# Kernel tuning notes

Hardware: AMD Instinct MI355X
Metric: run time of the kernel (lower is better)

Reference implementation:

```python
import jax, jax.numpy as jnp
import numpy as np

B, N, K, D, DEG = 16, 4096, 64, 128, 16  # graphs, nodes/graph, clusters, feat dim, avg degree
E = B * N * DEG


def setup_inputs() -> dict:
    key = jax.random.key(0)
    k0, k1, k2, k3, k4, k5 = jax.random.split(key, 6)
    x = jax.random.normal(k0, (B * N, D), dtype=jnp.float32)
    W = jax.random.normal(k1, (D, K), dtype=jnp.float32) / np.sqrt(D)
    b = jnp.zeros((K,), dtype=jnp.float32)
    # edges strictly within each graph, then offset by graph start
    offs = (jnp.arange(B) * N)[:, None]                      # [B,1]
    src = jax.random.randint(k2, (B, N * DEG), 0, N) + offs  # [B, N*DEG]
    dst = jax.random.randint(k3, (B, N * DEG), 0, N) + offs
    edge_index = jnp.stack([src.reshape(-1), dst.reshape(-1)], axis=0)  # [2,E]
    edge_weight = jax.random.uniform(k4, (E,), dtype=jnp.float32)
    batch_ptr = jnp.arange(B + 1, dtype=jnp.int64) * N
    # pre-sampled uniforms for gumbel noise (constant across fwd/bwd like torch)
    gumbel_u = jax.random.uniform(k5, (B * N, K), dtype=jnp.float32, minval=1e-6, maxval=1.0)
    return {"x": x, "W": W, "b": b, "edge_weight": edge_weight, "gumbel_u": gumbel_u,
            "edge_index": edge_index, "batch_ptr": batch_ptr}


def reference(x, W, b, edge_weight, gumbel_u, edge_index, batch_ptr):
    Ntot, Dd = x.shape
    Kk = W.shape[1]
    Bn = batch_ptr.shape[0] - 1
    Nn = Ntot // Bn  # equal-sized graphs

    # pooling net + hard gumbel-softmax (tau=1, straight-through)
    logits = x @ W + b                                   # [Ntot,K]
    g = -jnp.log(-jnp.log(gumbel_u))
    y_soft = jax.nn.softmax(logits + g, axis=-1)
    y_hard = jax.nn.one_hot(jnp.argmax(y_soft, axis=-1), Kk, dtype=y_soft.dtype)
    s = y_hard + y_soft - jax.lax.stop_gradient(y_soft)  # forward == one-hot

    sb = s.reshape(Bn, Nn, Kk)
    xb = x.reshape(Bn, Nn, Dd)
    out = jnp.einsum('bnk,bnd->bkd', sb, xb).reshape(Bn * Kk, Dd)

    src, dst = edge_index[0], edge_index[1]
    # A @ S via scatter over src, then S^T (A S) per graph
    AS = jax.ops.segment_sum(edge_weight[:, None] * s[dst], src, num_segments=Ntot)  # [Ntot,K]
    out_adj = jnp.einsum('bnk,bnl->bkl', sb, AS.reshape(Bn, Nn, Kk))                 # [B,K,K]

    # link loss: ||A - S S^T||_F per graph = sqrt(||A||^2 - 2<A,SS^T> + ||S^T S||^2)
    ge = src // Nn                                        # graph id per edge
    a_sq = jax.ops.segment_sum(edge_weight ** 2, ge, num_segments=Bn)
    cross = jax.ops.segment_sum(edge_weight * jnp.einsum('ek,ek->e', s[src], s[dst]), ge, num_segments=Bn)
    StS = jnp.einsum('bnk,bnl->bkl', sb, sb)
    sst_sq = jnp.sum(StS ** 2, axis=(1, 2))
    e_per = jax.ops.segment_sum(jnp.ones_like(edge_weight), ge, num_segments=Bn)
    link = jnp.sqrt(jnp.maximum(a_sq - 2.0 * cross + sst_sq, 0.0)) / e_per  # normalize=True
    link_loss = jnp.mean(link)

    ent = (-s * jnp.log(s + 1e-15)).sum(-1).reshape(Bn, Nn).mean(-1)
    entropy_loss = jnp.mean(ent)

    batch = jnp.repeat(jnp.arange(Bn), Kk)
    batch_ptr_out = jnp.arange(Bn + 1) * Kk
    return out, out_adj, link_loss, entropy_loss, batch, batch_ptr_out
```

## Files before the change

kernel.cpp:

```cpp
#include <hip/hip_runtime.h>

#define NGRAPH 16
#define NPG    4096
#define KCL    64
#define DF     128
#define NTOT   (NGRAPH*NPG)
#define NEDGE  (NTOT*16)



__global__ __launch_bounds__(256) void assign_kernel(
    const float* __restrict__ x, const float* __restrict__ W,
    const float* __restrict__ bias, const float* __restrict__ gum,
    unsigned char* __restrict__ clus)
{
    __shared__ __align__(16) float xs[64 * 132];
    __shared__ float cand_v[4][64];
    __shared__ int   cand_k[4][64];

    const int tid  = threadIdx.x;
    const int wave = tid >> 6;
    const int lane = tid & 63;
    const int n0   = blockIdx.x * 64;

    {
        const float4* xg = (const float4*)(x + (size_t)n0 * DF);
        #pragma unroll
        for (int i = 0; i < 8; ++i) {
            int j4 = tid + i * 256;
            int j  = j4 << 2;
            float4 v = xg[j4];
            *(float4*)&xs[(j >> 7) * 132 + (j & 127)] = v;
        }
    }
    __syncthreads();

    const int n  = lane;
    const int k0 = __builtin_amdgcn_readfirstlane(wave << 4);

    float acc[16];
    #pragma unroll
    for (int kk = 0; kk < 16; ++kk) acc[kk] = bias[k0 + kk];

    #pragma unroll 4
    for (int dc = 0; dc < 32; ++dc) {
        float4 xv = *(const float4*)&xs[n * 132 + (dc << 2)];
        const float* wp = W + (dc << 8) + k0;
        #pragma unroll
        for (int kk = 0; kk < 16; ++kk) {
            float a = acc[kk];
            a = fmaf(xv.x, wp[kk],        a);
            a = fmaf(xv.y, wp[64  + kk],  a);
            a = fmaf(xv.z, wp[128 + kk],  a);
            a = fmaf(xv.w, wp[192 + kk],  a);
            acc[kk] = a;
        }
    }

    const float* gp = gum + ((size_t)(n0 + n) << 6) + k0;
    float best = -3.4e38f; int bestk = k0;
    #pragma unroll
    for (int q = 0; q < 4; ++q) {
        float4 u = *(const float4*)(gp + (q << 2));
        float uv[4] = {u.x, u.y, u.z, u.w};
        #pragma unroll
        for (int r = 0; r < 4; ++r) {
            float g = -__logf(-__logf(uv[r]));
            float v = acc[(q << 2) + r] + g;
            if (v > best) { best = v; bestk = k0 + (q << 2) + r; }
        }
    }
    cand_v[wave][n] = best;
    cand_k[wave][n] = bestk;
    __syncthreads();

    if (tid < 64) {
        float bv = cand_v[0][tid]; int bk = cand_k[0][tid];
        #pragma unroll
        for (int w2 = 1; w2 < 4; ++w2) {
            float v = cand_v[w2][tid];
            if (v > bv) { bv = v; bk = cand_k[w2][tid]; }
        }
        clus[n0 + tid] = (unsigned char)bk;
    }
}

__global__ __launch_bounds__(1024) void sort_kernel(
    const unsigned char* __restrict__ clus,
    int* __restrict__ counts, int* __restrict__ starts,
    unsigned short* __restrict__ order)
{
    __shared__ int hist[KCL];
    __shared__ int offs[KCL];

    const int tid = threadIdx.x;
    const int bg  = blockIdx.x;

    if (tid < KCL) hist[tid] = 0;
    __syncthreads();

    unsigned char c[4];
    #pragma unroll
    for (int i = 0; i < 4; ++i) {
        c[i] = clus[(bg << 12) + tid + (i << 10)];
        atomicAdd(&hist[c[i]], 1);
    }
    __syncthreads();

    if (tid < KCL) {
        int v = hist[tid];
        int inc = v;
        #pragma unroll
        for (int off = 1; off < 64; off <<= 1) {
            int t = __shfl_up(inc, off);
            if (tid >= off) inc += t;
        }
        int excl = inc - v;
        offs[tid] = excl;
        counts[(bg << 6) + tid] = v;
        starts[(bg << 6) + tid] = excl;
    }
    __syncthreads();

    #pragma unroll
    for (int i = 0; i < 4; ++i) {
        int p = atomicAdd(&offs[c[i]], 1);
        order[(bg << 12) + p] = (unsigned short)(tid + (i << 10));
    }
}

__global__ __launch_bounds__(256) void pool_kernel(
    const float* __restrict__ x, const unsigned short* __restrict__ order,
    const int* __restrict__ counts, const int* __restrict__ starts,
    float* __restrict__ out)
{
    __shared__ unsigned short ord[NPG];
    __shared__ float4 part[8][32];

    const int tid   = threadIdx.x;
    const int bg    = blockIdx.x >> 6;
    const int k     = blockIdx.x & 63;
    const int cnt   = counts[(bg << 6) + k];
    const int start = starts[(bg << 6) + k];

    for (int i = tid; i < cnt; i += 256)
        ord[i] = order[(bg << 12) + start + i];
    __syncthreads();

    const int grp = tid >> 5;
    const int l32 = tid & 31;
    float4 acc = {0.0f, 0.0f, 0.0f, 0.0f};
    for (int i = grp; i < cnt; i += 8) {
        const float4* row = (const float4*)(x + ((size_t)(bg << 12) + ord[i]) * DF);
        float4 v = row[l32];
        acc.x += v.x; acc.y += v.y; acc.z += v.z; acc.w += v.w;
    }
    part[grp][l32] = acc;
    __syncthreads();

    if (grp == 0) {
        float4 s = part[0][l32];
        #pragma unroll
        for (int g = 1; g < 8; ++g) {
            float4 p = part[g][l32];
            s.x += p.x; s.y += p.y; s.z += p.z; s.w += p.w;
        }
        ((float4*)(out + (size_t)(bg << 13) + (k << 7)))[l32] = s;
    }
}

__global__ __launch_bounds__(512) void edge_kernel(
    const int* __restrict__ ei, const float* __restrict__ ew,
    const unsigned char* __restrict__ clus,
    float* __restrict__ out_adj, float* __restrict__ cross,
    float* __restrict__ asq)
{
    __shared__ float adj[KCL * KCL];
    __shared__ unsigned char cl[NPG];
    __shared__ float redc[8], redq[8];

    const int tid = threadIdx.x;
    const int bg  = blockIdx.x >> 2;
    const int q   = blockIdx.x & 3;

    #pragma unroll
    for (int i = 0; i < 8; ++i) adj[tid + i * 512] = 0.0f;
    #pragma unroll
    for (int i = 0; i < 2; ++i)
        ((int*)cl)[tid + i * 512] = ((const int*)(clus + (size_t)bg * NPG))[tid + i * 512];
    __syncthreads();

    const int e0 = bg * 65536 + q * 16384;
    float csum = 0.0f, qsum = 0.0f;

    #pragma unroll 4
    for (int it = 0; it < 32; ++it) {
        const int e = e0 + it * 512 + tid;
        const int s = ei[e]         & (NPG - 1);
        const int d = ei[NEDGE + e] & (NPG - 1);
        const float w = ew[e];
        const int ks = cl[s];
        const int kd = cl[d];
        atomicAdd(&adj[(ks << 6) + kd], w);
        csum += (ks == kd) ? w : 0.0f;
        qsum += w * w;
    }

    #pragma unroll
    for (int off = 32; off > 0; off >>= 1) {
        csum += __shfl_down(csum, off);
        qsum += __shfl_down(qsum, off);
    }
    const int lane = tid & 63, wv = tid >> 6;
    if (lane == 0) { redc[wv] = csum; redq[wv] = qsum; }
    __syncthreads();
    if (tid == 0) {
        float cs = 0.0f, qs = 0.0f;
        #pragma unroll
        for (int i = 0; i < 8; ++i) { cs += redc[i]; qs += redq[i]; }
        atomicAdd(&cross[bg], cs);
        atomicAdd(&asq[bg],  qs);
    }

    #pragma unroll
    for (int i = 0; i < 8; ++i) {
        const int j = tid + i * 512;
        atomicAdd(&out_adj[(bg << 12) + j], adj[j]);
    }
}

__global__ __launch_bounds__(1024) void finalize_kernel(
    const int* __restrict__ counts, const float* __restrict__ cross,
    const float* __restrict__ asq, float* __restrict__ out)
{
    __shared__ float links[16];
    const int tid = threadIdx.x;
    const int wv = tid >> 6, lane = tid & 63;

    float c  = (float)counts[(wv << 6) + lane];
    float s2 = c * c;
    #pragma unroll
    for (int off = 32; off > 0; off >>= 1) s2 += __shfl_down(s2, off);
    if (lane == 0) {
        float v = asq[wv] - 2.0f * cross[wv] + s2;
        links[wv] = sqrtf(fmaxf(v, 0.0f)) * (1.0f / 65536.0f);
    }
    __syncthreads();
    if (tid == 0) {
        float m = 0.0f;
        #pragma unroll
        for (int i = 0; i < 16; ++i) m += links[i];
        out[196608] = m * (1.0f / 16.0f);
        out[196609] = 0.0f;
    }
    out[196610 + tid] = (float)(tid >> 6);
    if (tid < 17) out[197634 + tid] = (float)(tid * 64);
}

extern "C" void kernel_launch(void* const* d_in, const int* in_sizes, int n_in,
                              void* d_out, int out_size, void* d_ws, size_t ws_size,
                              hipStream_t stream) {
    const float* x    = (const float*)d_in[0];
    const float* W    = (const float*)d_in[1];
    const float* bias = (const float*)d_in[2];
    const float* ew   = (const float*)d_in[3];
    const float* gum  = (const float*)d_in[4];
    const int*   ei   = (const int*)  d_in[5];

    float* out = (float*)d_out;

    unsigned char*  clus   = (unsigned char*) d_ws;
    int*            counts = (int*)           ((char*)d_ws + 65536);
    int*            starts = (int*)           ((char*)d_ws + 69632);
    float*          cross  = (float*)         ((char*)d_ws + 73728);
    float*          asq    = (float*)         ((char*)d_ws + 73792);
    unsigned short* order  = (unsigned short*)((char*)d_ws + 73856);

    hipMemsetAsync(out + 131072, 0, (size_t)65536 * sizeof(float), stream);
    hipMemsetAsync((char*)d_ws + 73728, 0, 128, stream);

    assign_kernel<<<NTOT / 64, 256, 0, stream>>>(x, W, bias, gum, clus);

    sort_kernel<<<NGRAPH, 1024, 0, stream>>>(clus, counts, starts, order);

    pool_kernel<<<NGRAPH * KCL, 256, 0, stream>>>(x, order, counts, starts, out);

    edge_kernel<<<NGRAPH * 4, 512, 0, stream>>>(
        ei, ew, clus, out + 131072, cross, asq);

    finalize_kernel<<<1, 1024, 0, stream>>>(counts, cross, asq, out);
}
```

Baseline: 156.5 us.

## Split edge kernel into more blocks and reduce partial adjacency in finalize

```diff
diff --git a/kernel.cpp b/kernel.cpp
--- a/kernel.cpp
+++ b/kernel.cpp
@@ -172,16 +172,16 @@
 __global__ __launch_bounds__(512) void edge_kernel(
     const int* __restrict__ ei, const float* __restrict__ ew,
     const unsigned char* __restrict__ clus,
-    float* __restrict__ out_adj, float* __restrict__ cross,
-    float* __restrict__ asq)
+    float* __restrict__ partials, float* __restrict__ crossp,
+    float* __restrict__ asqp)
 {
     __shared__ float adj[KCL * KCL];
     __shared__ unsigned char cl[NPG];
     __shared__ float redc[8], redq[8];
 
     const int tid = threadIdx.x;
-    const int bg  = blockIdx.x >> 2;
-    const int q   = blockIdx.x & 3;
+    const int bg  = blockIdx.x >> 4;
+    const int sl  = blockIdx.x & 15;
 
     #pragma unroll
     for (int i = 0; i < 8; ++i) adj[tid + i * 512] = 0.0f;
@@ -190,11 +190,11 @@
         ((int*)cl)[tid + i * 512] = ((const int*)(clus + (size_t)bg * NPG))[tid + i * 512];
     __syncthreads();
 
-    const int e0 = bg * 65536 + q * 16384;
+    const int e0 = bg * 65536 + sl * 4096;
     float csum = 0.0f, qsum = 0.0f;
 
-    #pragma unroll 4
-    for (int it = 0; it < 32; ++it) {
+    #pragma unroll
+    for (int it = 0; it < 8; ++it) {
         const int e = e0 + it * 512 + tid;
         const int s = ei[e]         & (NPG - 1);
         const int d = ei[NEDGE + e] & (NPG - 1);
@@ -214,35 +214,57 @@
     const int lane = tid & 63, wv = tid >> 6;
     if (lane == 0) { redc[wv] = csum; redq[wv] = qsum; }
     __syncthreads();
+
     if (tid == 0) {
         float cs = 0.0f, qs = 0.0f;
         #pragma unroll
         for (int i = 0; i < 8; ++i) { cs += redc[i]; qs += redq[i]; }
-        atomicAdd(&cross[bg], cs);
-        atomicAdd(&asq[bg],  qs);
-    }
-
-    #pragma unroll
-    for (int i = 0; i < 8; ++i) {
-        const int j = tid + i * 512;
-        atomicAdd(&out_adj[(bg << 12) + j], adj[j]);
-    }
-}
-
-__global__ __launch_bounds__(1024) void finalize_kernel(
-    const int* __restrict__ counts, const float* __restrict__ cross,
-    const float* __restrict__ asq, float* __restrict__ out)
-{
+        crossp[blockIdx.x] = cs;
+        asqp[blockIdx.x]   = qs;
+    }
+
+    float4*       dst = (float4*)(partials + (size_t)blockIdx.x * 4096);
+    const float4* src = (const float4*)adj;
+    dst[tid]       = src[tid];
+    dst[tid + 512] = src[tid + 512];
+}
+
+__global__ __launch_bounds__(1024) void reduce_finalize_kernel(
+    const float* __restrict__ partials, const float* __restrict__ crossp,
+    const float* __restrict__ asqp, const int* __restrict__ counts,
+    float* __restrict__ out)
+{
+    const int tid = threadIdx.x;
+
+    if (blockIdx.x < 64) {
+        const int cell = blockIdx.x * 1024 + tid;
+        const int bg   = cell >> 12;
+        const int j    = cell & 4095;
+        float s = 0.0f;
+        #pragma unroll
+        for (int sl = 0; sl < 16; ++sl)
+            s += partials[(size_t)((bg << 4) + sl) * 4096 + j];
+        out[131072 + cell] = s;
+        return;
+    }
+
     __shared__ float links[16];
-    const int tid = threadIdx.x;
     const int wv = tid >> 6, lane = tid & 63;
 
     float c  = (float)counts[(wv << 6) + lane];
     float s2 = c * c;
     #pragma unroll
     for (int off = 32; off > 0; off >>= 1) s2 += __shfl_down(s2, off);
+
+    float cp = (lane < 16) ? crossp[(wv << 4) + lane] : 0.0f;
+    float ap = (lane < 16) ? asqp[(wv << 4) + lane]   : 0.0f;
+    #pragma unroll
+    for (int off = 8; off > 0; off >>= 1) {
+        cp += __shfl_down(cp, off);
+        ap += __shfl_down(ap, off);
+    }
     if (lane == 0) {
-        float v = asq[wv] - 2.0f * cross[wv] + s2;
+        float v = ap - 2.0f * cp + s2;
         links[wv] = sqrtf(fmaxf(v, 0.0f)) * (1.0f / 65536.0f);
     }
     __syncthreads();
@@ -269,15 +291,14 @@
 
     float* out = (float*)d_out;
 
-    unsigned char*  clus   = (unsigned char*) d_ws;
-    int*            counts = (int*)           ((char*)d_ws + 65536);
-    int*            starts = (int*)           ((char*)d_ws + 69632);
-    float*          cross  = (float*)         ((char*)d_ws + 73728);
-    float*          asq    = (float*)         ((char*)d_ws + 73792);
-    unsigned short* order  = (unsigned short*)((char*)d_ws + 73856);
-
-    hipMemsetAsync(out + 131072, 0, (size_t)65536 * sizeof(float), stream);
-    hipMemsetAsync((char*)d_ws + 73728, 0, 128, stream);
+    unsigned char*  clus     = (unsigned char*) d_ws;
+    int*            counts   = (int*)           ((char*)d_ws + 65536);
+    int*            starts   = (int*)           ((char*)d_ws + 69632);
+    float*          crossp   = (float*)         ((char*)d_ws + 73728);
+    float*          asqp     = (float*)         ((char*)d_ws + 74752);
+    unsigned short* order    = (unsigned short*)((char*)d_ws + 75776);
+    float*          partials = (float*)         ((char*)d_ws + 206848);
+
 
     assign_kernel<<<NTOT / 64, 256, 0, stream>>>(x, W, bias, gum, clus);
 
@@ -285,8 +306,9 @@
 
     pool_kernel<<<NGRAPH * KCL, 256, 0, stream>>>(x, order, counts, starts, out);
 
-    edge_kernel<<<NGRAPH * 4, 512, 0, stream>>>(
-        ei, ew, clus, out + 131072, cross, asq);
-
-    finalize_kernel<<<1, 1024, 0, stream>>>(counts, cross, asq, out);
-}
+    edge_kernel<<<NGRAPH * 16, 512, 0, stream>>>(
+        ei, ew, clus, partials, crossp, asqp);
+
+    reduce_finalize_kernel<<<65, 1024, 0, stream>>>(
+        partials, crossp, asqp, counts, out);
+}
```

New measurement: 136.2 us. -13.0%, faster.

## Merge sort+edge and pool+finalize kernels, replace atomics with partial reductions

Applied to the files above, without the earlier changes.

```diff
diff --git a/kernel.cpp b/kernel.cpp
--- a/kernel.cpp
+++ b/kernel.cpp
@@ -4,10 +4,17 @@
 #define NPG    4096
 #define KCL    64
 #define DF     128
-#define NTOT   (NGRAPH*NPG)
-#define NEDGE  (NTOT*16)
-
-
+#define NTOT   65536
+#define NEDGE  1048576
+
+
+#define WS_CLUS   0
+#define WS_CNT    65536
+#define WS_START  69632
+#define WS_CROSS  73728
+#define WS_ASQ    74752
+#define WS_ORDER  75776
+#define WS_ADJP   206848
 
 __global__ __launch_bounds__(256) void assign_kernel(
     const float* __restrict__ x, const float* __restrict__ W,
@@ -18,33 +25,28 @@
     __shared__ float cand_v[4][64];
     __shared__ int   cand_k[4][64];
 
-    const int tid  = threadIdx.x;
-    const int wave = tid >> 6;
-    const int lane = tid & 63;
-    const int n0   = blockIdx.x * 64;
+    const int tid = threadIdx.x, wave = tid >> 6, lane = tid & 63;
+    const int n0 = blockIdx.x * 64;
 
     {
         const float4* xg = (const float4*)(x + (size_t)n0 * DF);
         #pragma unroll
         for (int i = 0; i < 8; ++i) {
-            int j4 = tid + i * 256;
-            int j  = j4 << 2;
+            int j4 = tid + i * 256; int j = j4 << 2;
             float4 v = xg[j4];
             *(float4*)&xs[(j >> 7) * 132 + (j & 127)] = v;
         }
     }
     __syncthreads();
 
-    const int n  = lane;
     const int k0 = __builtin_amdgcn_readfirstlane(wave << 4);
-
     float acc[16];
     #pragma unroll
     for (int kk = 0; kk < 16; ++kk) acc[kk] = bias[k0 + kk];
 
     #pragma unroll 4
     for (int dc = 0; dc < 32; ++dc) {
-        float4 xv = *(const float4*)&xs[n * 132 + (dc << 2)];
+        float4 xv = *(const float4*)&xs[lane * 132 + (dc << 2)];
         const float* wp = W + (dc << 8) + k0;
         #pragma unroll
         for (int kk = 0; kk < 16; ++kk) {
@@ -57,7 +59,7 @@
         }
     }
 
-    const float* gp = gum + ((size_t)(n0 + n) << 6) + k0;
+    const float* gp = gum + ((size_t)(n0 + lane) << 6) + k0;
     float best = -3.4e38f; int bestk = k0;
     #pragma unroll
     for (int q = 0; q < 4; ++q) {
@@ -70,8 +72,8 @@
             if (v > best) { best = v; bestk = k0 + (q << 2) + r; }
         }
     }
-    cand_v[wave][n] = best;
-    cand_k[wave][n] = bestk;
+    cand_v[wave][lane] = best;
+    cand_k[wave][lane] = bestk;
     __syncthreads();
 
     if (tid < 64) {
@@ -85,176 +87,167 @@
     }
 }
 
-__global__ __launch_bounds__(1024) void sort_kernel(
+__global__ __launch_bounds__(1024) void sortedge_kernel(
     const unsigned char* __restrict__ clus,
+    const int* __restrict__ ei, const float* __restrict__ ew,
     int* __restrict__ counts, int* __restrict__ starts,
-    unsigned short* __restrict__ order)
+    unsigned short* __restrict__ order,
+    float* __restrict__ adjp, float* __restrict__ crossp,
+    float* __restrict__ asqp)
 {
-    __shared__ int hist[KCL];
-    __shared__ int offs[KCL];
+    __shared__ int   hist[KCL];
+    __shared__ int   offs[KCL];
+    __shared__ float adj[KCL * KCL];
+    __shared__ unsigned char cl[NPG];
+    __shared__ float redc[16], redq[16];
 
     const int tid = threadIdx.x;
-    const int bg  = blockIdx.x;
-
-    if (tid < KCL) hist[tid] = 0;
-    __syncthreads();
-
-    unsigned char c[4];
-    #pragma unroll
-    for (int i = 0; i < 4; ++i) {
-        c[i] = clus[(bg << 12) + tid + (i << 10)];
-        atomicAdd(&hist[c[i]], 1);
-    }
-    __syncthreads();
-
-    if (tid < KCL) {
-        int v = hist[tid];
-        int inc = v;
-        #pragma unroll
-        for (int off = 1; off < 64; off <<= 1) {
-            int t = __shfl_up(inc, off);
-            if (tid >= off) inc += t;
-        }
-        int excl = inc - v;
-        offs[tid] = excl;
-        counts[(bg << 6) + tid] = v;
-        starts[(bg << 6) + tid] = excl;
-    }
-    __syncthreads();
-
-    #pragma unroll
-    for (int i = 0; i < 4; ++i) {
-        int p = atomicAdd(&offs[c[i]], 1);
-        order[(bg << 12) + p] = (unsigned short)(tid + (i << 10));
-    }
-}
-
-__global__ __launch_bounds__(256) void pool_kernel(
+
+    if (blockIdx.x < 16) {
+        const int bg = blockIdx.x;
+        if (tid < KCL) hist[tid] = 0;
+        __syncthreads();
+        unsigned char c[4];
+        #pragma unroll
+        for (int i = 0; i < 4; ++i) {
+            c[i] = clus[(bg << 12) + tid + (i << 10)];
+            atomicAdd(&hist[c[i]], 1);
+        }
+        __syncthreads();
+        if (tid < KCL) {
+            int v = hist[tid], inc = v;
+            #pragma unroll
+            for (int off = 1; off < 64; off <<= 1) {
+                int t = __shfl_up(inc, off);
+                if (tid >= off) inc += t;
+            }
+            int excl = inc - v;
+            offs[tid] = excl;
+            counts[(bg << 6) + tid] = v;
+            starts[(bg << 6) + tid] = excl;
+        }
+        __syncthreads();
+        #pragma unroll
+        for (int i = 0; i < 4; ++i) {
+            int p = atomicAdd(&offs[c[i]], 1);
+            order[(bg << 12) + p] = (unsigned short)(tid + (i << 10));
+        }
+    } else {
+        const int eb = blockIdx.x - 16;
+        const int bg = eb >> 4;
+        ((float4*)adj)[tid] = make_float4(0.f, 0.f, 0.f, 0.f);
+        ((int*)cl)[tid] = ((const int*)(clus + (size_t)bg * NPG))[tid];
+        __syncthreads();
+
+        const int e0 = eb << 12;
+        float csum = 0.f, qsum = 0.f;
+        #pragma unroll
+        for (int it = 0; it < 4; ++it) {
+            const int e = e0 + (it << 10) + tid;
+            const int s = ei[e]         & (NPG - 1);
+            const int d = ei[NEDGE + e] & (NPG - 1);
+            const float w = ew[e];
+            const int ks = cl[s], kd = cl[d];
+            atomicAdd(&adj[(ks << 6) + kd], w);
+            csum += (ks == kd) ? w : 0.f;
+            qsum += w * w;
+        }
+        #pragma unroll
+        for (int off = 32; off > 0; off >>= 1) {
+            csum += __shfl_down(csum, off);
+            qsum += __shfl_down(qsum, off);
+        }
+        const int lane = tid & 63, wv = tid >> 6;
+        if (lane == 0) { redc[wv] = csum; redq[wv] = qsum; }
+        __syncthreads();
+        if (tid == 0) {
+            float cs = 0.f, qs = 0.f;
+            #pragma unroll
+            for (int i = 0; i < 16; ++i) { cs += redc[i]; qs += redq[i]; }
+            crossp[eb] = cs;
+            asqp[eb]   = qs;
+        }
+        ((float4*)(adjp + ((size_t)eb << 12)))[tid] = ((const float4*)adj)[tid];
+    }
+}
+
+__global__ __launch_bounds__(256) void poolreduce_kernel(
     const float* __restrict__ x, const unsigned short* __restrict__ order,
     const int* __restrict__ counts, const int* __restrict__ starts,
-    float* __restrict__ out)
+    const float* __restrict__ adjp, const float* __restrict__ crossp,
+    const float* __restrict__ asqp, float* __restrict__ out)
 {
     __shared__ unsigned short ord[NPG];
     __shared__ float4 part[8][32];
-
-    const int tid   = threadIdx.x;
-    const int bg    = blockIdx.x >> 6;
-    const int k     = blockIdx.x & 63;
-    const int cnt   = counts[(bg << 6) + k];
-    const int start = starts[(bg << 6) + k];
-
-    for (int i = tid; i < cnt; i += 256)
-        ord[i] = order[(bg << 12) + start + i];
-    __syncthreads();
-
-    const int grp = tid >> 5;
-    const int l32 = tid & 31;
-    float4 acc = {0.0f, 0.0f, 0.0f, 0.0f};
-    for (int i = grp; i < cnt; i += 8) {
-        const float4* row = (const float4*)(x + ((size_t)(bg << 12) + ord[i]) * DF);
-        float4 v = row[l32];
-        acc.x += v.x; acc.y += v.y; acc.z += v.z; acc.w += v.w;
-    }
-    part[grp][l32] = acc;
-    __syncthreads();
-
-    if (grp == 0) {
-        float4 s = part[0][l32];
-        #pragma unroll
-        for (int g = 1; g < 8; ++g) {
-            float4 p = part[g][l32];
-            s.x += p.x; s.y += p.y; s.z += p.z; s.w += p.w;
-        }
-        ((float4*)(out + (size_t)(bg << 13) + (k << 7)))[l32] = s;
-    }
-}
-
-__global__ __launch_bounds__(512) void edge_kernel(
-    const int* __restrict__ ei, const float* __restrict__ ew,
-    const unsigned char* __restrict__ clus,
-    float* __restrict__ out_adj, float* __restrict__ cross,
-    float* __restrict__ asq)
-{
-    __shared__ float adj[KCL * KCL];
-    __shared__ unsigned char cl[NPG];
-    __shared__ float redc[8], redq[8];
+    __shared__ float links[16];
 
     const int tid = threadIdx.x;
-    const int bg  = blockIdx.x >> 2;
-    const int q   = blockIdx.x & 3;
-
-    #pragma unroll
-    for (int i = 0; i < 8; ++i) adj[tid + i * 512] = 0.0f;
-    #pragma unroll
-    for (int i = 0; i < 2; ++i)
-        ((int*)cl)[tid + i * 512] = ((const int*)(clus + (size_t)bg * NPG))[tid + i * 512];
-    __syncthreads();
-
-    const int e0 = bg * 65536 + q * 16384;
-    float csum = 0.0f, qsum = 0.0f;
-
-    #pragma unroll 4
-    for (int it = 0; it < 32; ++it) {
-        const int e = e0 + it * 512 + tid;
-        const int s = ei[e]         & (NPG - 1);
-        const int d = ei[NEDGE + e] & (NPG - 1);
-        const float w = ew[e];
-        const int ks = cl[s];
-        const int kd = cl[d];
-        atomicAdd(&adj[(ks << 6) + kd], w);
-        csum += (ks == kd) ? w : 0.0f;
-        qsum += w * w;
-    }
-
-    #pragma unroll
-    for (int off = 32; off > 0; off >>= 1) {
-        csum += __shfl_down(csum, off);
-        qsum += __shfl_down(qsum, off);
-    }
-    const int lane = tid & 63, wv = tid >> 6;
-    if (lane == 0) { redc[wv] = csum; redq[wv] = qsum; }
-    __syncthreads();
-    if (tid == 0) {
-        float cs = 0.0f, qs = 0.0f;
-        #pragma unroll
-        for (int i = 0; i < 8; ++i) { cs += redc[i]; qs += redq[i]; }
-        atomicAdd(&cross[bg], cs);
-        atomicAdd(&asq[bg],  qs);
-    }
-
-    #pragma unroll
-    for (int i = 0; i < 8; ++i) {
-        const int j = tid + i * 512;
-        atomicAdd(&out_adj[(bg << 12) + j], adj[j]);
-    }
-}
-
-__global__ __launch_bounds__(1024) void finalize_kernel(
-    const int* __restrict__ counts, const float* __restrict__ cross,
-    const float* __restrict__ asq, float* __restrict__ out)
-{
-    __shared__ float links[16];
-    const int tid = threadIdx.x;
-    const int wv = tid >> 6, lane = tid & 63;
-
-    float c  = (float)counts[(wv << 6) + lane];
-    float s2 = c * c;
-    #pragma unroll
-    for (int off = 32; off > 0; off >>= 1) s2 += __shfl_down(s2, off);
-    if (lane == 0) {
-        float v = asq[wv] - 2.0f * cross[wv] + s2;
-        links[wv] = sqrtf(fmaxf(v, 0.0f)) * (1.0f / 65536.0f);
-    }
-    __syncthreads();
-    if (tid == 0) {
-        float m = 0.0f;
-        #pragma unroll
-        for (int i = 0; i < 16; ++i) m += links[i];
-        out[196608] = m * (1.0f / 16.0f);
-        out[196609] = 0.0f;
-    }
-    out[196610 + tid] = (float)(tid >> 6);
-    if (tid < 17) out[197634 + tid] = (float)(tid * 64);
+    const int blk = blockIdx.x;
+
+    if (blk < 1024) {
+        const int bg = blk >> 6, k = blk & 63;
+        const int cnt = counts[blk], start = starts[blk];
+        for (int i = tid; i < cnt; i += 256)
+            ord[i] = order[(bg << 12) + start + i];
+        __syncthreads();
+        const int grp = tid >> 5, l32 = tid & 31;
+        float4 acc = {0.f, 0.f, 0.f, 0.f};
+        for (int i = grp; i < cnt; i += 8) {
+            const float4* row = (const float4*)(x + (((size_t)(bg << 12) + ord[i]) << 7));
+            float4 v = row[l32];
+            acc.x += v.x; acc.y += v.y; acc.z += v.z; acc.w += v.w;
+        }
+        part[grp][l32] = acc;
+        __syncthreads();
+        if (grp == 0) {
+            float4 s = part[0][l32];
+            #pragma unroll
+            for (int g = 1; g < 8; ++g) {
+                float4 p = part[g][l32];
+                s.x += p.x; s.y += p.y; s.z += p.z; s.w += p.w;
+            }
+            ((float4*)(out + ((size_t)(bg << 13) + (k << 7))))[l32] = s;
+        }
+    } else if (blk < 1280) {
+        const int cell = ((blk - 1024) << 8) + tid;
+        const int bg = cell >> 12, j = cell & 4095;
+        float s = 0.f;
+        #pragma unroll
+        for (int sl = 0; sl < 16; ++sl)
+            s += adjp[(size_t)(((bg << 4) + sl) << 12) + j];
+        out[131072 + cell] = s;
+    } else {
+        if (tid < 16) {
+            const int bg = tid;
+            float s2 = 0.f;
+            #pragma unroll 8
+            for (int k = 0; k < 64; ++k) {
+                float c = (float)counts[(bg << 6) + k];
+                s2 = fmaf(c, c, s2);
+            }
+            float cs = 0.f, as = 0.f;
+            #pragma unroll
+            for (int sl = 0; sl < 16; ++sl) {
+                cs += crossp[(bg << 4) + sl];
+                as += asqp[(bg << 4) + sl];
+            }
+            links[bg] = sqrtf(fmaxf(as - 2.f * cs + s2, 0.f)) * (1.f / 65536.f);
+        }
+        __syncthreads();
+        if (tid == 0) {
+            float m = 0.f;
+            #pragma unroll
+            for (int i = 0; i < 16; ++i) m += links[i];
+            out[196608] = m * (1.f / 16.f);
+            out[196609] = 0.f;
+        }
+        #pragma unroll
+        for (int r = 0; r < 4; ++r) {
+            int i = tid + (r << 8);
+            out[196610 + i] = (float)(i >> 6);
+        }
+        if (tid < 17) out[197634 + tid] = (float)(tid << 6);
+    }
 }
 
 extern "C" void kernel_launch(void* const* d_in, const int* in_sizes, int n_in,
@@ -268,25 +261,21 @@
     const int*   ei   = (const int*)  d_in[5];
 
     float* out = (float*)d_out;
-
-    unsigned char*  clus   = (unsigned char*) d_ws;
-    int*            counts = (int*)           ((char*)d_ws + 65536);
-    int*            starts = (int*)           ((char*)d_ws + 69632);
-    float*          cross  = (float*)         ((char*)d_ws + 73728);
-    float*          asq    = (float*)         ((char*)d_ws + 73792);
-    unsigned short* order  = (unsigned short*)((char*)d_ws + 73856);
-
-    hipMemsetAsync(out + 131072, 0, (size_t)65536 * sizeof(float), stream);
-    hipMemsetAsync((char*)d_ws + 73728, 0, 128, stream);
+    char*  wsb = (char*)d_ws;
+
+    unsigned char*  clus   = (unsigned char*) (wsb + WS_CLUS);
+    int*            counts = (int*)           (wsb + WS_CNT);
+    int*            starts = (int*)           (wsb + WS_START);
+    float*          crossp = (float*)         (wsb + WS_CROSS);
+    float*          asqp   = (float*)         (wsb + WS_ASQ);
+    unsigned short* order  = (unsigned short*)(wsb + WS_ORDER);
+    float*          adjp   = (float*)         (wsb + WS_ADJP);
 
     assign_kernel<<<NTOT / 64, 256, 0, stream>>>(x, W, bias, gum, clus);
 
-    sort_kernel<<<NGRAPH, 1024, 0, stream>>>(clus, counts, starts, order);
-
-    pool_kernel<<<NGRAPH * KCL, 256, 0, stream>>>(x, order, counts, starts, out);
-
-    edge_kernel<<<NGRAPH * 4, 512, 0, stream>>>(
-        ei, ew, clus, out + 131072, cross, asq);
-
-    finalize_kernel<<<1, 1024, 0, stream>>>(counts, cross, asq, out);
-}
+    sortedge_kernel<<<16 + 256, 1024, 0, stream>>>(
+        clus, ei, ew, counts, starts, order, adjp, crossp, asqp);
+
+    poolreduce_kernel<<<1024 + 256 + 1, 256, 0, stream>>>(
+        x, order, counts, starts, adjp, crossp, asqp, out);
+}
```

Result: faster. 128.7 us (-17.7%).
